# Kernel optimization log

Hardware: AMD Instinct MI355X
Metric: run time of the kernel (lower is better)

## Reference

```python
import jax, jax.numpy as jnp
import numpy as np

T_SCHEDULE = 999.0
LOG_2PI = float(np.log(2.0 * np.pi))


def setup_inputs() -> dict:
    key = jax.random.key(0)
    k1, k2, k3 = jax.random.split(key, 3)
    xt = jax.random.normal(k1, (128, 3, 32, 32), dtype=jnp.float32)
    # integer-style diffusion timesteps in [0, 900); divided by t_schedule=999 inside
    t = jax.random.uniform(k2, (128,), dtype=jnp.float32) * 900.0
    gt_images = jax.random.normal(k3, (20000, 3, 32, 32), dtype=jnp.float32)
    return {"xt": xt, "t": t, "gt_images": gt_images}


def reference(xt, t, gt_images):
    # AnalyticFlow.forward_fast
    B = xt.shape[0]
    N = gt_images.shape[0]
    x = jax.lax.stop_gradient(xt.reshape(B, -1))  # original detaches x
    gt = gt_images.reshape(N, -1)                 # [N, D]
    D = x.shape[-1]
    tt = t / T_SCHEDULE                           # [B]
    sig = 1.0 - tt                                # [B]
    # log N(term_2; 0, I) summed over D, where term_2 = (x - t*gt)/(1-t).
    # ||x - t*gt||^2 = ||x||^2 - 2 t x.gt + t^2 ||gt||^2  (avoids B*N*D tensor)
    x2 = jnp.sum(x * x, axis=-1)                  # [B]
    g2 = jnp.sum(gt * gt, axis=-1)                # [N]
    xg = x @ gt.T                                 # [B, N] GEMM
    sq = x2[:, None] - 2.0 * tt[:, None] * xg + (tt * tt)[:, None] * g2[None, :]
    log_p = -0.5 * sq / (sig * sig)[:, None] - 0.5 * D * LOG_2PI  # [B, N]
    log_p = log_p - jnp.max(log_p)                # global-max shift as in original
    eta = jax.nn.softmax(log_p, axis=1)           # [B, N], rows sum to 1
    # drift = mean_n (N*eta_n) * (gt_n - x)/(1-t) = (eta @ gt - x)/(1-t)
    drift = (eta @ gt - x) / sig[:, None]         # [B, D]
    return drift.reshape(xt.shape)
```

## Files before the change

### kernel.cpp

```cpp
#include <hip/hip_runtime.h>
#include <hip/hip_bf16.h>
#include <stdint.h>

#define B_SZ   128
#define D_SZ   3072
#define N_SZ   20000
#define NPAD   20480
#define BN     (B_SZ * NPAD)
#define BD     (B_SZ * D_SZ)

typedef __attribute__((ext_vector_type(8))) short        short8;
typedef __attribute__((ext_vector_type(4))) float        f32x4;
typedef __attribute__((ext_vector_type(2))) unsigned int uint2v;

__device__ __forceinline__ unsigned short f2bf(float f) {
    unsigned u = __float_as_uint(f);
    u += 0x7FFFu + ((u >> 16) & 1u);
    return (unsigned short)(u >> 16);
}
__device__ __forceinline__ float bf2f(unsigned short h) {
    return __uint_as_float(((unsigned)h) << 16);
}
__device__ __forceinline__ unsigned pk2bf(float a, float b) {
    __hip_bfloat162 h = __float22bfloat162_rn(make_float2(a, b));
    unsigned r;
    __builtin_memcpy(&r, &h, 4);
    return r;
}
__device__ __forceinline__ unsigned fkey_enc(float f) {
    unsigned b = __float_as_uint(f);
    return (b & 0x80000000u) ? ~b : (b | 0x80000000u);
}
__device__ __forceinline__ float fkey_dec(unsigned u) {
    return __uint_as_float((u & 0x80000000u) ? (u ^ 0x80000000u) : ~u);
}

__device__ __forceinline__ void gl_lds16(const void* g, void* l) {
    __builtin_amdgcn_global_load_lds(
        (const __attribute__((address_space(1))) void*)g,
        (__attribute__((address_space(3))) void*)l, 16, 0, 0);
}

__device__ __forceinline__ int swz(int r, int q) { return q ^ ((r >> 1) & 3); }

__global__ __launch_bounds__(256) void zero_small(float* __restrict__ p)
{
    p[blockIdx.x * 256 + threadIdx.x] = 0.f;
}

__global__ __launch_bounds__(256) void prep_x(const float* __restrict__ x,
                                              unsigned short* __restrict__ xhi,
                                              unsigned short* __restrict__ xlo)
{
    int i = blockIdx.x * 256 + threadIdx.x;
    float v = x[i];
    unsigned short h = f2bf(v);
    xhi[i] = h;
    xlo[i] = f2bf(v - bf2f(h));
}

__global__ __launch_bounds__(256) void scores_kernel(
        const float* __restrict__ gt,
        const unsigned short* __restrict__ xhi,
        const unsigned short* __restrict__ xlo,
        float* __restrict__ XG_part,
        float* __restrict__ G2)
{
    __shared__ __align__(16) unsigned short Xhi_t[128 * 32];
    __shared__ __align__(16) unsigned short Xlo_t[128 * 32];
    __shared__ __align__(16) unsigned short Ghi_t[64 * 32];
    __shared__ __align__(16) unsigned short Glo_t[64 * 32];

    const int tid   = threadIdx.x;
    const int kc    = blockIdx.x & 7;
    const int nt    = blockIdx.x >> 3;
    const int nbase = nt * 64;
    const int kcb   = kc * 384;

    const int lane = tid & 63;
    const int wave = tid >> 6;
    const int mh = wave & 1;
    const int nh = wave >> 1;
    const int lm = lane & 15;
    const int qd = lane >> 4;

    const int gn = tid >> 2;
    const int gq = tid & 3;
    const int ng0 = nbase + gn;
    int grow = ng0 > N_SZ - 1 ? N_SZ - 1 : ng0;
    const float* gp0 = gt + (size_t)grow * D_SZ + kcb + gq * 8;
    const int gwr = gn * 32 + swz(gn, gq) * 8;

    int xsrc[2], xdst[2];
    #pragma unroll
    for (int i = 0; i < 2; i++) {
        int o = (i * 256 + tid) * 16;
        int r = o >> 6;
        int j = (o >> 4) & 3;
        xdst[i] = o;
        xsrc[i] = r * D_SZ + kcb + swz(r, j) * 8;
    }

    float g2acc = 0.0f;

    f32x4 acc[4][2];
    #pragma unroll
    for (int i = 0; i < 4; i++)
        #pragma unroll
        for (int j = 0; j < 2; j++)
            acc[i][j] = (f32x4){0.f, 0.f, 0.f, 0.f};

    for (int k0 = 0; k0 < 384; k0 += 32) {
        #pragma unroll
        for (int i = 0; i < 2; i++) {
            gl_lds16(xhi + xsrc[i] + k0, (char*)Xhi_t + xdst[i]);
            gl_lds16(xlo + xsrc[i] + k0, (char*)Xlo_t + xdst[i]);
        }
        f32x4 v0 = *(const f32x4*)(gp0 + k0);
        f32x4 v1 = *(const f32x4*)(gp0 + k0 + 4);
        short8 h8, l8;
        #pragma unroll
        for (int j = 0; j < 4; j++) {
            float a = v0[j], b = v1[j];
            unsigned short ha = f2bf(a), hb = f2bf(b);
            h8[j]     = (short)ha;  h8[j + 4] = (short)hb;
            l8[j]     = (short)f2bf(a - bf2f(ha));
            l8[j + 4] = (short)f2bf(b - bf2f(hb));
            g2acc += a * a + b * b;
        }
        *(short8*)&Ghi_t[gwr] = h8;
        *(short8*)&Glo_t[gwr] = l8;

        __syncthreads();

        short8 bhi[2], blo[2];
        #pragma unroll
        for (int ni = 0; ni < 2; ni++) {
            int r = nh * 32 + ni * 16 + lm;
            int sl = r * 32 + swz(r, qd) * 8;
            bhi[ni] = *(short8*)&Ghi_t[sl];
            blo[ni] = *(short8*)&Glo_t[sl];
        }
        #pragma unroll
        for (int mi = 0; mi < 4; mi++) {
            int r = mh * 64 + mi * 16 + lm;
            int sl = r * 32 + swz(r, qd) * 8;
            short8 ahi = *(short8*)&Xhi_t[sl];
            short8 alo = *(short8*)&Xlo_t[sl];
            #pragma unroll
            for (int ni = 0; ni < 2; ni++) {
                acc[mi][ni] = __builtin_amdgcn_mfma_f32_16x16x32_bf16(ahi, bhi[ni], acc[mi][ni], 0, 0, 0);
                acc[mi][ni] = __builtin_amdgcn_mfma_f32_16x16x32_bf16(ahi, blo[ni], acc[mi][ni], 0, 0, 0);
                acc[mi][ni] = __builtin_amdgcn_mfma_f32_16x16x32_bf16(alo, bhi[ni], acc[mi][ni], 0, 0, 0);
            }
        }
        __syncthreads();
    }

    g2acc += __shfl_xor(g2acc, 1);
    g2acc += __shfl_xor(g2acc, 2);
    if (gq == 0 && ng0 < N_SZ) atomicAdd(&G2[ng0], g2acc);

    float* XGp = XG_part + (size_t)kc * BN;
    #pragma unroll
    for (int mi = 0; mi < 4; mi++) {
        #pragma unroll
        for (int ni = 0; ni < 2; ni++) {
            int ncol = nh * 32 + ni * 16 + lm;
            int ng = nbase + ncol;
            if (ng < N_SZ) {
                #pragma unroll
                for (int i = 0; i < 4; i++) {
                    int m = mh * 64 + mi * 16 + qd * 4 + i;
                    XGp[(size_t)m * NPAD + ng] = acc[mi][ni][i];
                }
            }
        }
    }
}

__global__ __launch_bounds__(256) void sum8(
        const float* __restrict__ XG_part, float* __restrict__ XG)
{
    int i = (blockIdx.x * 256 + threadIdx.x) * 4;
    f32x4 s = (f32x4){0.f, 0.f, 0.f, 0.f};
    #pragma unroll
    for (int kc = 0; kc < 8; kc++)
        s += *(const f32x4*)(XG_part + (size_t)kc * BN + i);
    *(f32x4*)(XG + i) = s;
}

__global__ __launch_bounds__(256) void maxk(
        const float* __restrict__ XG, const float* __restrict__ G2,
        const float* __restrict__ tarr, unsigned* __restrict__ Mkey)
{
    const int b  = blockIdx.x >> 3;
    const int ch = blockIdx.x & 7;
    const int tid = threadIdx.x;
    float tt  = tarr[b] / 999.0f;
    float sig = 1.0f - tt;
    float inv = 1.0f / (sig * sig);
    float c1 = tt * inv, c2 = 0.5f * tt * tt * inv;
    const float* xg = XG + (size_t)b * NPAD;
    __shared__ float wred[4];

    float mx = -3.402823466e+38f;
    int n0 = ch * 2560;
    for (int n = n0 + tid; n < n0 + 2560; n += 256)
        if (n < N_SZ) mx = fmaxf(mx, c1 * xg[n] - c2 * G2[n]);
    #pragma unroll
    for (int o = 32; o > 0; o >>= 1) mx = fmaxf(mx, __shfl_xor(mx, o));
    if ((tid & 63) == 0) wred[tid >> 6] = mx;
    __syncthreads();
    if (tid == 0) {
        mx = fmaxf(fmaxf(wred[0], wred[1]), fmaxf(wred[2], wred[3]));
        atomicMax(&Mkey[b], fkey_enc(mx));
    }
}

__global__ __launch_bounds__(256) void expk(
        const float* __restrict__ XG, const float* __restrict__ G2,
        const float* __restrict__ tarr, const unsigned* __restrict__ Mkey,
        unsigned short* __restrict__ P, float* __restrict__ L)
{
    const int b  = blockIdx.x >> 3;
    const int ch = blockIdx.x & 7;
    const int tid = threadIdx.x;
    float tt  = tarr[b] / 999.0f;
    float sig = 1.0f - tt;
    float inv = 1.0f / (sig * sig);
    float c1 = tt * inv, c2 = 0.5f * tt * tt * inv;
    float m = fkey_dec(Mkey[b]);
    const float* xg = XG + (size_t)b * NPAD;
    unsigned short* prow = P + (size_t)b * NPAD;
    __shared__ float wred[4];

    float sum = 0.f;
    int n0 = ch * 2560;
    for (int n = n0 + tid; n < n0 + 2560; n += 256) {
        float p = 0.f;
        if (n < N_SZ) { p = expf(c1 * xg[n] - c2 * G2[n] - m); sum += p; }
        prow[n] = f2bf(p);
    }
    #pragma unroll
    for (int o = 32; o > 0; o >>= 1) sum += __shfl_xor(sum, o);
    if ((tid & 63) == 0) wred[tid >> 6] = sum;
    __syncthreads();
    if (tid == 0) atomicAdd(&L[b], wred[0] + wred[1] + wred[2] + wred[3]);
}

__global__ __launch_bounds__(256) void drift_kernel(
        const float* __restrict__ gt,
        const unsigned short* __restrict__ P,
        float* __restrict__ Dacc_part)
{
    __shared__ __align__(16) unsigned short Pt[128 * 32];
    __shared__ __align__(16) unsigned short Gt[128 * 40];

    const int tid = threadIdx.x;
    const int nt = blockIdx.x % 24;
    const int kc = blockIdx.x / 24;
    const int dbase = nt * 128;

    const int lane = tid & 63;
    const int wave = tid >> 6;
    const int mh = wave & 1;
    const int dh = wave >> 1;
    const int lm = lane & 15;
    const int qd = lane >> 4;

    const int dg = tid & 31;
    const int kq = tid >> 5;

    int psrc[2], pdst[2];
    #pragma unroll
    for (int i = 0; i < 2; i++) {
        int o = (i * 256 + tid) * 16;
        int r = o >> 6;
        int j = (o >> 4) & 3;
        pdst[i] = o;
        psrc[i] = r * NPAD + kc * 512 + swz(r, j) * 8;
    }

    f32x4 acc[4][4];
    #pragma unroll
    for (int i = 0; i < 4; i++)
        #pragma unroll
        for (int j = 0; j < 4; j++)
            acc[i][j] = (f32x4){0.f, 0.f, 0.f, 0.f};

    for (int s = 0; s < 16; s++) {
        int kb = kc * 512 + s * 32;
        #pragma unroll
        for (int i = 0; i < 2; i++)
            gl_lds16(P + psrc[i] + s * 32, (char*)Pt + pdst[i]);
        f32x4 row[4];
        #pragma unroll
        for (int i = 0; i < 4; i++) {
            int kg = kb + kq * 4 + i;
            if (kg > N_SZ - 1) kg = N_SZ - 1;
            row[i] = *(const f32x4*)(gt + (size_t)kg * D_SZ + dbase + dg * 4);
        }
        #pragma unroll
        for (int j = 0; j < 4; j++) {
            unsigned u01 = pk2bf(row[0][j], row[1][j]);
            unsigned u23 = pk2bf(row[2][j], row[3][j]);
            uint2v pk = (uint2v){u01, u23};
            __builtin_memcpy((char*)Gt + (size_t)(dg * 4 + j) * 80 + kq * 8, &pk, 8);
        }
        __syncthreads();

        short8 af[4], bf8[4];
        #pragma unroll
        for (int mi = 0; mi < 4; mi++) {
            int r = mh * 64 + mi * 16 + lm;
            af[mi] = *(short8*)&Pt[r * 32 + swz(r, qd) * 8];
        }
        #pragma unroll
        for (int ni = 0; ni < 4; ni++)
            bf8[ni] = *(short8*)((char*)Gt + (size_t)(dh * 64 + ni * 16 + lm) * 80 + qd * 16);
        #pragma unroll
        for (int mi = 0; mi < 4; mi++)
            #pragma unroll
            for (int ni = 0; ni < 4; ni++)
                acc[mi][ni] = __builtin_amdgcn_mfma_f32_16x16x32_bf16(af[mi], bf8[ni], acc[mi][ni], 0, 0, 0);
        __syncthreads();
    }

    float* Dp = Dacc_part + (size_t)kc * BD;
    #pragma unroll
    for (int mi = 0; mi < 4; mi++)
        #pragma unroll
        for (int ni = 0; ni < 4; ni++) {
            int d = dbase + dh * 64 + ni * 16 + lm;
            #pragma unroll
            for (int i = 0; i < 4; i++) {
                int m = mh * 64 + mi * 16 + qd * 4 + i;
                Dp[(size_t)m * D_SZ + d] = acc[mi][ni][i];
            }
        }
}

__global__ __launch_bounds__(256) void epilogue_kernel(
        const float* __restrict__ Dacc_part, const float* __restrict__ L,
        const float* __restrict__ x, const float* __restrict__ tarr,
        float* __restrict__ out)
{
    int i = (blockIdx.x * 256 + threadIdx.x) * 4;
    int b = i / D_SZ;
    f32x4 s = (f32x4){0.f, 0.f, 0.f, 0.f};
    #pragma unroll
    for (int kc = 0; kc < 40; kc++)
        s += *(const f32x4*)(Dacc_part + (size_t)kc * BD + i);
    float tt = tarr[b] / 999.0f;
    float sig = 1.0f - tt;
    float invL = 1.0f / L[b];
    f32x4 xv = *(const f32x4*)(x + i);
    f32x4 o;
    #pragma unroll
    for (int j = 0; j < 4; j++) o[j] = (s[j] * invL - xv[j]) / sig;
    *(f32x4*)(out + i) = o;
}

extern "C" void kernel_launch(void* const* d_in, const int* in_sizes, int n_in,
                              void* d_out, int out_size, void* d_ws, size_t ws_size,
                              hipStream_t stream)
{
    const float* xt = (const float*)d_in[0];
    const float* t  = (const float*)d_in[1];
    const float* gt = (const float*)d_in[2];
    float* out = (float*)d_out;

    char* ws = (char*)d_ws;
    float*          XG_part  = (float*)(ws + 0);
    float*          XG       = (float*)(ws + 83886080);
    float*          Dacc_part= (float*)(ws + 94371840);
    float*          G2       = (float*)(ws + 157286400);
    unsigned*       Mkey     = (unsigned*)(ws + 157368320);
    float*          L        = (float*)(ws + 157368832);
    unsigned short* Xhi      = (unsigned short*)(ws + 157369344);
    unsigned short* Xlo      = (unsigned short*)(ws + 158155776);
    unsigned short* P        = (unsigned short*)(ws + 158942208);

    zero_small    <<<   81, 256, 0, stream>>>(G2);
    prep_x        <<< 1536, 256, 0, stream>>>(xt, Xhi, Xlo);
    scores_kernel <<< 2504, 256, 0, stream>>>(gt, Xhi, Xlo, XG_part, G2);
    sum8          <<< 2560, 256, 0, stream>>>(XG_part, XG);
    maxk          <<< 1024, 256, 0, stream>>>(XG, G2, t, Mkey);
    expk          <<< 1024, 256, 0, stream>>>(XG, G2, t, Mkey, P, L);
    drift_kernel  <<<  960, 256, 0, stream>>>(gt, P, Dacc_part);
    epilogue_kernel<<< 384, 256, 0, stream>>>(Dacc_part, L, xt, t, out);
}
```

Before: 486.8 us.

## Halve split-K, emit bf16 gt copy for drift, fuse sum with max

The scores kernel now uses 4 K-chunks instead of 8 and writes the bf16-high part of gt to a workspace buffer, which the drift kernel reads in place of fp32 gt. This halves gt read traffic in the drift GEMM and removes its in-loop conversion. The split-K partial sum is fused with the row-max reduction, so one launch and one full pass over XG go away. Drift also uses 20 K-chunks instead of 40, which shrinks partial buffers and epilogue reduction traffic. Fewer blocks may reduce occupancy in scores and drift, and the extra bf16 store adds write traffic in scores.

```diff
diff --git a/kernel.cpp b/kernel.cpp
--- a/kernel.cpp
+++ b/kernel.cpp
@@ -8,10 +8,13 @@
 #define NPAD   20480
 #define BN     (B_SZ * NPAD)
 #define BD     (B_SZ * D_SZ)
-
-typedef __attribute__((ext_vector_type(8))) short        short8;
-typedef __attribute__((ext_vector_type(4))) float        f32x4;
-typedef __attribute__((ext_vector_type(2))) unsigned int uint2v;
+#define KC_S   4
+#define KC_D   20
+
+typedef __attribute__((ext_vector_type(8))) short          short8;
+typedef __attribute__((ext_vector_type(4))) float          f32x4;
+typedef __attribute__((ext_vector_type(4))) unsigned short u16x4;
+typedef __attribute__((ext_vector_type(2))) unsigned int   uint2v;
 
 __device__ __forceinline__ unsigned short f2bf(float f) {
     unsigned u = __float_as_uint(f);
@@ -20,12 +23,6 @@
 }
 __device__ __forceinline__ float bf2f(unsigned short h) {
     return __uint_as_float(((unsigned)h) << 16);
-}
-__device__ __forceinline__ unsigned pk2bf(float a, float b) {
-    __hip_bfloat162 h = __float22bfloat162_rn(make_float2(a, b));
-    unsigned r;
-    __builtin_memcpy(&r, &h, 4);
-    return r;
 }
 __device__ __forceinline__ unsigned fkey_enc(float f) {
     unsigned b = __float_as_uint(f);
@@ -64,7 +61,8 @@
         const unsigned short* __restrict__ xhi,
         const unsigned short* __restrict__ xlo,
         float* __restrict__ XG_part,
-        float* __restrict__ G2)
+        float* __restrict__ G2,
+        unsigned short* __restrict__ Gh)
 {
     __shared__ __align__(16) unsigned short Xhi_t[128 * 32];
     __shared__ __align__(16) unsigned short Xlo_t[128 * 32];
@@ -72,10 +70,10 @@
     __shared__ __align__(16) unsigned short Glo_t[64 * 32];
 
     const int tid   = threadIdx.x;
-    const int kc    = blockIdx.x & 7;
-    const int nt    = blockIdx.x >> 3;
+    const int kc    = blockIdx.x & 3;
+    const int nt    = blockIdx.x >> 2;
     const int nbase = nt * 64;
-    const int kcb   = kc * 384;
+    const int kcb   = kc * 768;
 
     const int lane = tid & 63;
     const int wave = tid >> 6;
@@ -89,6 +87,7 @@
     const int ng0 = nbase + gn;
     int grow = ng0 > N_SZ - 1 ? N_SZ - 1 : ng0;
     const float* gp0 = gt + (size_t)grow * D_SZ + kcb + gq * 8;
+    unsigned short* ghp0 = Gh + (size_t)ng0 * D_SZ + kcb + gq * 8;
     const int gwr = gn * 32 + swz(gn, gq) * 8;
 
     int xsrc[2], xdst[2];
@@ -110,7 +109,7 @@
         for (int j = 0; j < 2; j++)
             acc[i][j] = (f32x4){0.f, 0.f, 0.f, 0.f};
 
-    for (int k0 = 0; k0 < 384; k0 += 32) {
+    for (int k0 = 0; k0 < 768; k0 += 32) {
         #pragma unroll
         for (int i = 0; i < 2; i++) {
             gl_lds16(xhi + xsrc[i] + k0, (char*)Xhi_t + xdst[i]);
@@ -130,6 +129,7 @@
         }
         *(short8*)&Ghi_t[gwr] = h8;
         *(short8*)&Glo_t[gwr] = l8;
+        if (ng0 < N_SZ) *(short8*)(ghp0 + k0) = h8;
 
         __syncthreads();
 
@@ -179,35 +179,32 @@
     }
 }
 
-__global__ __launch_bounds__(256) void sum8(
-        const float* __restrict__ XG_part, float* __restrict__ XG)
-{
-    int i = (blockIdx.x * 256 + threadIdx.x) * 4;
+__global__ __launch_bounds__(256) void sum4max(
+        const float* __restrict__ XG_part, const float* __restrict__ G2,
+        const float* __restrict__ tarr, float* __restrict__ XG,
+        unsigned* __restrict__ Mkey)
+{
+    const int tid = threadIdx.x;
+    const int b = blockIdx.x / 20;
+    const int i = (blockIdx.x * 256 + tid) * 4;
+    __shared__ float wred[4];
+
     f32x4 s = (f32x4){0.f, 0.f, 0.f, 0.f};
     #pragma unroll
-    for (int kc = 0; kc < 8; kc++)
+    for (int kc = 0; kc < KC_S; kc++)
         s += *(const f32x4*)(XG_part + (size_t)kc * BN + i);
     *(f32x4*)(XG + i) = s;
-}
-
-__global__ __launch_bounds__(256) void maxk(
-        const float* __restrict__ XG, const float* __restrict__ G2,
-        const float* __restrict__ tarr, unsigned* __restrict__ Mkey)
-{
-    const int b  = blockIdx.x >> 3;
-    const int ch = blockIdx.x & 7;
-    const int tid = threadIdx.x;
+
     float tt  = tarr[b] / 999.0f;
     float sig = 1.0f - tt;
     float inv = 1.0f / (sig * sig);
     float c1 = tt * inv, c2 = 0.5f * tt * tt * inv;
-    const float* xg = XG + (size_t)b * NPAD;
-    __shared__ float wred[4];
+    int n = i - b * NPAD;
 
     float mx = -3.402823466e+38f;
-    int n0 = ch * 2560;
-    for (int n = n0 + tid; n < n0 + 2560; n += 256)
-        if (n < N_SZ) mx = fmaxf(mx, c1 * xg[n] - c2 * G2[n]);
+    #pragma unroll
+    for (int j = 0; j < 4; j++)
+        if (n + j < N_SZ) mx = fmaxf(mx, c1 * s[j] - c2 * G2[n + j]);
     #pragma unroll
     for (int o = 32; o > 0; o >>= 1) mx = fmaxf(mx, __shfl_xor(mx, o));
     if ((tid & 63) == 0) wred[tid >> 6] = mx;
@@ -250,7 +247,7 @@
 }
 
 __global__ __launch_bounds__(256) void drift_kernel(
-        const float* __restrict__ gt,
+        const unsigned short* __restrict__ Gh,
         const unsigned short* __restrict__ P,
         float* __restrict__ Dacc_part)
 {
@@ -279,7 +276,7 @@
         int r = o >> 6;
         int j = (o >> 4) & 3;
         pdst[i] = o;
-        psrc[i] = r * NPAD + kc * 512 + swz(r, j) * 8;
+        psrc[i] = r * NPAD + kc * 1024 + swz(r, j) * 8;
     }
 
     f32x4 acc[4][4];
@@ -289,22 +286,22 @@
         for (int j = 0; j < 4; j++)
             acc[i][j] = (f32x4){0.f, 0.f, 0.f, 0.f};
 
-    for (int s = 0; s < 16; s++) {
-        int kb = kc * 512 + s * 32;
+    for (int s = 0; s < 32; s++) {
+        int kb = kc * 1024 + s * 32;
         #pragma unroll
         for (int i = 0; i < 2; i++)
             gl_lds16(P + psrc[i] + s * 32, (char*)Pt + pdst[i]);
-        f32x4 row[4];
+        u16x4 row[4];
         #pragma unroll
         for (int i = 0; i < 4; i++) {
             int kg = kb + kq * 4 + i;
             if (kg > N_SZ - 1) kg = N_SZ - 1;
-            row[i] = *(const f32x4*)(gt + (size_t)kg * D_SZ + dbase + dg * 4);
+            row[i] = *(const u16x4*)(Gh + (size_t)kg * D_SZ + dbase + dg * 4);
         }
         #pragma unroll
         for (int j = 0; j < 4; j++) {
-            unsigned u01 = pk2bf(row[0][j], row[1][j]);
-            unsigned u23 = pk2bf(row[2][j], row[3][j]);
+            unsigned u01 = (unsigned)row[0][j] | ((unsigned)row[1][j] << 16);
+            unsigned u23 = (unsigned)row[2][j] | ((unsigned)row[3][j] << 16);
             uint2v pk = (uint2v){u01, u23};
             __builtin_memcpy((char*)Gt + (size_t)(dg * 4 + j) * 80 + kq * 8, &pk, 8);
         }
@@ -350,7 +347,7 @@
     int b = i / D_SZ;
     f32x4 s = (f32x4){0.f, 0.f, 0.f, 0.f};
     #pragma unroll
-    for (int kc = 0; kc < 40; kc++)
+    for (int kc = 0; kc < KC_D; kc++)
         s += *(const f32x4*)(Dacc_part + (size_t)kc * BD + i);
     float tt = tarr[b] / 999.0f;
     float sig = 1.0f - tt;
@@ -373,21 +370,21 @@
 
     char* ws = (char*)d_ws;
     float*          XG_part  = (float*)(ws + 0);
-    float*          XG       = (float*)(ws + 83886080);
-    float*          Dacc_part= (float*)(ws + 94371840);
-    float*          G2       = (float*)(ws + 157286400);
-    unsigned*       Mkey     = (unsigned*)(ws + 157368320);
-    float*          L        = (float*)(ws + 157368832);
-    unsigned short* Xhi      = (unsigned short*)(ws + 157369344);
-    unsigned short* Xlo      = (unsigned short*)(ws + 158155776);
-    unsigned short* P        = (unsigned short*)(ws + 158942208);
+    float*          XG       = (float*)(ws + 41943040);
+    float*          Dacc_part= (float*)(ws + 52428800);
+    float*          G2       = (float*)(ws + 83886080);
+    unsigned*       Mkey     = (unsigned*)(ws + 83968000);
+    float*          L        = (float*)(ws + 83968512);
+    unsigned short* Xhi      = (unsigned short*)(ws + 83969024);
+    unsigned short* Xlo      = (unsigned short*)(ws + 84755456);
+    unsigned short* P        = (unsigned short*)(ws + 85541888);
+    unsigned short* Gh       = (unsigned short*)(ws + 90784768);
 
     zero_small    <<<   81, 256, 0, stream>>>(G2);
     prep_x        <<< 1536, 256, 0, stream>>>(xt, Xhi, Xlo);
-    scores_kernel <<< 2504, 256, 0, stream>>>(gt, Xhi, Xlo, XG_part, G2);
-    sum8          <<< 2560, 256, 0, stream>>>(XG_part, XG);
-    maxk          <<< 1024, 256, 0, stream>>>(XG, G2, t, Mkey);
+    scores_kernel <<< 1252, 256, 0, stream>>>(gt, Xhi, Xlo, XG_part, G2, Gh);
+    sum4max       <<< 2560, 256, 0, stream>>>(XG_part, G2, t, XG, Mkey);
     expk          <<< 1024, 256, 0, stream>>>(XG, G2, t, Mkey, P, L);
-    drift_kernel  <<<  960, 256, 0, stream>>>(gt, P, Dacc_part);
+    drift_kernel  <<<  480, 256, 0, stream>>>(Gh, P, Dacc_part);
     epilogue_kernel<<< 384, 256, 0, stream>>>(Dacc_part, L, xt, t, out);
 }
```

Result: slower. 498.3 us (+2.4%).
